# Kernel optimization log

Hardware: AMD Instinct MI355X
Metric: run time of the kernel (lower is better)

The kernel has to match this reference:

```python
import jax, jax.numpy as jnp
import numpy as np

NDIM = 1024
NHEAD = 16
HEAD_DIM = NDIM // NHEAD


def setup_inputs() -> dict:
    key = jax.random.key(0)
    ks = jax.random.split(key, 12)
    B, L, C = 2, 2048, NDIM
    s = 0.02
    return {
        "q": jax.random.normal(ks[0], (B, L, C), jnp.float32),
        "k": jax.random.normal(ks[1], (B, L, C), jnp.float32),
        "v": jax.random.normal(ks[2], (B, L, C), jnp.float32),
        "Wq": jax.random.normal(ks[3], (C, C), jnp.float32) * s,
        "bq": jax.random.normal(ks[4], (C,), jnp.float32) * s,
        "Wk": jax.random.normal(ks[5], (C, C), jnp.float32) * s,
        "bk": jax.random.normal(ks[6], (C,), jnp.float32) * s,
        "Wv": jax.random.normal(ks[7], (C, C), jnp.float32) * s,
        "bv": jax.random.normal(ks[8], (C,), jnp.float32) * s,
        "Wo": jax.random.normal(ks[9], (C, C), jnp.float32) * s,
        "bo": jax.random.normal(ks[10], (C,), jnp.float32) * s,
    }


def reference(q, k, v, Wq, bq, Wk, bk, Wv, bv, Wo, bo):
    B, Lq, C = q.shape
    H, D = NHEAD, HEAD_DIM
    # projections, then split heads: (B, H, L, D)
    qh = (q @ Wq + bq).reshape(B, Lq, H, D).transpose(0, 2, 1, 3)
    kh = (k @ Wk + bk).reshape(B, k.shape[1], H, D).transpose(0, 2, 1, 3)
    vh = (v @ Wv + bv).reshape(B, v.shape[1], H, D).transpose(0, 2, 1, 3)
    scale = 1.0 / jnp.sqrt(jnp.asarray(D, qh.dtype))
    att = jnp.einsum("bhqd,bhkd->bhqk", qh, kh) * scale  # (B,H,Lq,Lk)
    att = jax.nn.softmax(att, axis=-1)  # dropout p=0.0 -> identity
    y = jnp.einsum("bhqk,bhkd->bhqd", att, vh)
    y = y.transpose(0, 2, 1, 3).reshape(B, Lq, C)
    return y @ Wo + bo
```

## Files before the change

kernel.cpp:

```cpp
#include <hip/hip_runtime.h>
#include <math.h>

#define BATCH 2
#define SEQ   2048
#define CDIM  1024
#define NHEAD 16
#define HDIM  64
#define TOKS  (BATCH * SEQ)

typedef __bf16 bf16x8 __attribute__((ext_vector_type(8)));
typedef __bf16 bf16x2 __attribute__((ext_vector_type(2)));
typedef float  f32x4  __attribute__((ext_vector_type(4)));

#define MFMA16(a, b, c) __builtin_amdgcn_mfma_f32_16x16x32_bf16(a, b, c, 0, 0, 0)

#define QSCALE 0.1803368801111204f

__device__ __forceinline__ void gload_lds16(const __bf16* g, __bf16* l) {
    __builtin_amdgcn_global_load_lds(
        (const __attribute__((address_space(1))) unsigned int*)g,
        (__attribute__((address_space(3))) unsigned int*)l, 16, 0, 0);
}

__global__ __launch_bounds__(256) void prep_kernel(
    const float* __restrict__ q, const float* __restrict__ k, const float* __restrict__ v,
    __bf16* __restrict__ qo, __bf16* __restrict__ ko, __bf16* __restrict__ vo,
    const float* __restrict__ W0, const float* __restrict__ W1,
    const float* __restrict__ W2, const float* __restrict__ W3,
    __bf16* __restrict__ T0, __bf16* __restrict__ T1,
    __bf16* __restrict__ T2, __bf16* __restrict__ T3)
{
    __shared__ __bf16 Ts[64][72];
    const int bx = blockIdx.x;
    const int tid = threadIdx.x;

    if (bx < 6144) {
        const int t = bx >> 11;
        const size_t i = ((size_t)(bx & 2047) * 256 + tid) * 8;
        const float* s = t == 0 ? q : (t == 1 ? k : v);
        __bf16* d = t == 0 ? qo : (t == 1 ? ko : vo);
        const float4 x = *(const float4*)&s[i];
        const float4 y = *(const float4*)&s[i + 4];
        bf16x8 o;
        o[0] = (__bf16)x.x; o[1] = (__bf16)x.y; o[2] = (__bf16)x.z; o[3] = (__bf16)x.w;
        o[4] = (__bf16)y.x; o[5] = (__bf16)y.y; o[6] = (__bf16)y.z; o[7] = (__bf16)y.w;
        *(bf16x8*)&d[i] = o;
        return;
    }

    const int t  = bx - 6144;
    const int z  = t >> 8;
    const int ry = (t & 255) >> 4;
    const int rx = t & 15;
    const float* W = z == 0 ? W0 : z == 1 ? W1 : z == 2 ? W2 : W3;
    __bf16* T = z == 0 ? T0 : z == 1 ? T1 : z == 2 ? T2 : T3;
    const int rb = ry * 64, cb = rx * 64;
    const int r = tid >> 4;
    const int c4 = (tid & 15) * 4;
#pragma unroll
    for (int p = 0; p < 4; p++) {
        const int rr = p * 16 + r;
        const float4 w4 = *(const float4*)&W[(size_t)(rb + rr) * CDIM + cb + c4];
        Ts[c4 + 0][rr] = (__bf16)w4.x;
        Ts[c4 + 1][rr] = (__bf16)w4.y;
        Ts[c4 + 2][rr] = (__bf16)w4.z;
        Ts[c4 + 3][rr] = (__bf16)w4.w;
    }
    __syncthreads();
    const int n = tid >> 2;
    const int k16 = (tid & 3) * 16;
    *(bf16x8*)&T[(size_t)(cb + n) * CDIM + rb + k16]     = *(const bf16x8*)&Ts[n][k16];
    *(bf16x8*)&T[(size_t)(cb + n) * CDIM + rb + k16 + 8] = *(const bf16x8*)&Ts[n][k16 + 8];
}

__global__ __launch_bounds__(512, 6) void qkv_gemm_kernel(
    const __bf16* __restrict__ qb, const __bf16* __restrict__ kb,
    const __bf16* __restrict__ vb,
    const __bf16* __restrict__ Wqt, const __bf16* __restrict__ Wkt,
    const __bf16* __restrict__ Wvt,
    const float* __restrict__ bq, const float* __restrict__ bk,
    const float* __restrict__ bv,
    __bf16* __restrict__ Qh, __bf16* __restrict__ Kh, __bf16* __restrict__ Vht)
{
    __shared__ __bf16 As[128 * 32];
    __shared__ __bf16 Bs[128 * 32];

    const int lin = blockIdx.x + (blockIdx.y << 3) + (blockIdx.z << 8);
    const int nl  = (lin & 7) * 96 + (lin >> 3);
    const int bx  = nl & 7;
    const int by  = (nl >> 3) & 31;
    const int z   = nl >> 8;

    const __bf16* A    = z == 0 ? qb : z == 1 ? kb : Wvt;
    const __bf16* Bt   = z == 0 ? Wqt : z == 1 ? Wkt : vb;
    const float*  bias = z == 0 ? bq : z == 1 ? bk : bv;

    const int tid  = threadIdx.x;
    const int w    = tid >> 6;
    const int lane = tid & 63;
    const int quad = lane >> 4;
    const int c    = lane & 15;
    const int wm   = w >> 1;
    const int wn   = w & 1;
    const int rowBase = (z == 2 ? bx : by) * 128;
    const int colBase = (z == 2 ? by : bx) * 128;

    const int sr = lane >> 2;
    const int sk = (lane & 3) * 8;

    f32x4 acc[2][4];
#pragma unroll
    for (int i = 0; i < 2; i++)
#pragma unroll
        for (int j = 0; j < 4; j++) acc[i][j] = (f32x4){0, 0, 0, 0};

    const __bf16* srcA = A  + (size_t)(rowBase + w * 16 + sr) * CDIM + sk;
    const __bf16* srcB = Bt + (size_t)(colBase + w * 16 + sr) * CDIM + sk;
    __bf16* dstA = &As[w * 16 * 32];
    __bf16* dstB = &Bs[w * 16 * 32];

    for (int k0 = 0; k0 < CDIM; k0 += 32) {
        gload_lds16(srcA + k0, dstA);
        gload_lds16(srcB + k0, dstB);
        __syncthreads();

        bf16x8 af[2], bf[4];
#pragma unroll
        for (int i = 0; i < 2; i++)
            af[i] = *(const bf16x8*)&As[(wm * 32 + i * 16 + c) * 32 + quad * 8];
#pragma unroll
        for (int i = 0; i < 4; i++)
            bf[i] = *(const bf16x8*)&Bs[(wn * 64 + i * 16 + c) * 32 + quad * 8];
#pragma unroll
        for (int mi = 0; mi < 2; mi++)
#pragma unroll
            for (int ni = 0; ni < 4; ni++)
                acc[mi][ni] = MFMA16(af[mi], bf[ni], acc[mi][ni]);
        __syncthreads();
    }

#pragma unroll
    for (int mi = 0; mi < 2; mi++) {
#pragma unroll
        for (int ni = 0; ni < 4; ni++) {
            const int col = colBase + wn * 64 + ni * 16 + c;
#pragma unroll
            for (int r = 0; r < 4; r++) {
                const int row = rowBase + wm * 32 + mi * 16 + quad * 4 + r;
                const float val = acc[mi][ni][r];
                if (z == 2) {
                    const int col2 = (col & ~31) | (((col & 15) << 1) | ((col >> 4) & 1));
                    Vht[(size_t)row * TOKS + col2] = (__bf16)(val + bias[row]);
                } else {
                    const int b = row >> 11, l = row & 2047;
                    const int h = col >> 6,  d = col & 63;
                    const float s = (z == 0) ? QSCALE : 1.0f;
                    __bf16* outp = (z == 0) ? Qh : Kh;
                    outp[((((size_t)b * NHEAD + h) * SEQ) + l) * HDIM + d] =
                        (__bf16)((val + bias[col]) * s);
                }
            }
        }
    }
}

__global__ __launch_bounds__(512, 4) void out_gemm_kernel(
    const __bf16* __restrict__ A, const __bf16* __restrict__ Bt,
    const float* __restrict__ bias, float* __restrict__ out)
{
    __shared__ __bf16 As[128 * 32];
    __shared__ __bf16 Bs[64 * 32];

    const int lin = blockIdx.x + (blockIdx.y << 4);
    const int nl  = (lin & 7) * 64 + (lin >> 3);
    const int bx  = nl & 15;
    const int by  = nl >> 4;

    const int tid  = threadIdx.x;
    const int w    = tid >> 6;
    const int lane = tid & 63;
    const int quad = lane >> 4;
    const int c    = lane & 15;
    const int wm   = w >> 1;
    const int wn   = w & 1;
    const int rowBase = by * 128;
    const int colBase = bx * 64;
    const int sr = lane >> 2;
    const int sk = (lane & 3) * 8;

    f32x4 acc[2][2];
#pragma unroll
    for (int i = 0; i < 2; i++)
#pragma unroll
        for (int j = 0; j < 2; j++) acc[i][j] = (f32x4){0, 0, 0, 0};

    const __bf16* srcA = A + (size_t)(rowBase + w * 16 + sr) * CDIM + sk;
    const __bf16* srcB = Bt + (size_t)(colBase + (w & 3) * 16 + sr) * CDIM + sk;
    __bf16* dstA = &As[w * 16 * 32];
    __bf16* dstB = &Bs[(w & 3) * 16 * 32];

    for (int k0 = 0; k0 < CDIM; k0 += 32) {
        gload_lds16(srcA + k0, dstA);
        if (w < 4) gload_lds16(srcB + k0, dstB);
        __syncthreads();

        bf16x8 af[2], bf[2];
#pragma unroll
        for (int i = 0; i < 2; i++)
            af[i] = *(const bf16x8*)&As[(wm * 32 + i * 16 + c) * 32 + quad * 8];
#pragma unroll
        for (int i = 0; i < 2; i++)
            bf[i] = *(const bf16x8*)&Bs[(wn * 32 + i * 16 + c) * 32 + quad * 8];
#pragma unroll
        for (int mi = 0; mi < 2; mi++)
#pragma unroll
            for (int ni = 0; ni < 2; ni++)
                acc[mi][ni] = MFMA16(af[mi], bf[ni], acc[mi][ni]);
        __syncthreads();
    }

#pragma unroll
    for (int mi = 0; mi < 2; mi++) {
#pragma unroll
        for (int ni = 0; ni < 2; ni++) {
            const int col = colBase + wn * 32 + ni * 16 + c;
#pragma unroll
            for (int r = 0; r < 4; r++) {
                const int row = rowBase + wm * 32 + mi * 16 + quad * 4 + r;
                out[(size_t)row * CDIM + col] = acc[mi][ni][r] + bias[col];
            }
        }
    }
}

__global__ __launch_bounds__(256) void attn_v5_kernel(
    const __bf16* __restrict__ Qh, const __bf16* __restrict__ Kh,
    const __bf16* __restrict__ Vht, __bf16* __restrict__ Y)
{
    __shared__ __align__(16) __bf16 Ks[2][32][72];
    __shared__ __align__(16) __bf16 Vt[2][64][48];
    __shared__ __align__(16) unsigned int Pf[4][2][16][36];

    const int tid  = threadIdx.x;
    const int w    = tid >> 6;
    const int lane = tid & 63;
    const int quad = lane >> 4;
    const int c    = lane & 15;
    const int bh   = blockIdx.x;
    const int b    = bh >> 4;
    const int h    = bh & 15;
    const int qbase = blockIdx.y * 128 + w * 32;

    const __bf16* Qg = Qh + (size_t)bh * SEQ * HDIM;
    const __bf16* Kg = Kh + (size_t)bh * SEQ * HDIM;
    const __bf16* Vg = Vht + (size_t)(h * HDIM) * TOKS + (size_t)b * SEQ;

    bf16x8 qf[2][2];
#pragma unroll
    for (int g = 0; g < 2; g++) {
        qf[g][0] = *(const bf16x8*)&Qg[(size_t)(qbase + g * 16 + c) * HDIM + quad * 8];
        qf[g][1] = *(const bf16x8*)&Qg[(size_t)(qbase + g * 16 + c) * HDIM + 32 + quad * 8];
    }

    bf16x8 ones;
#pragma unroll
    for (int j = 0; j < 8; j++) ones[j] = (__bf16)1.0f;

    f32x4 O[2][4];
    f32x4 L[2];
#pragma unroll
    for (int g = 0; g < 2; g++) {
        L[g] = (f32x4){0, 0, 0, 0};
#pragma unroll
        for (int i = 0; i < 4; i++) O[g][i] = (f32x4){0, 0, 0, 0};
    }

    const int krow = tid >> 3, kcol = (tid & 7) * 8;
    const int vrow = tid >> 2, vcol = (tid & 3) * 8;

    {
        const bf16x8 k0 = *(const bf16x8*)&Kg[(size_t)krow * HDIM + kcol];
        const bf16x8 v0 = *(const bf16x8*)&Vg[(size_t)vrow * TOKS + vcol];
        *(bf16x8*)&Ks[0][krow][kcol] = k0;
        *(bf16x8*)&Vt[0][vrow][vcol] = v0;
    }
    __syncthreads();

    int buf = 0;
    for (int t0 = 0; t0 < SEQ; t0 += 32) {
        const int tn = t0 + 32;
        bf16x8 kpre, vpre;
        if (tn < SEQ) {
            kpre = *(const bf16x8*)&Kg[(size_t)(tn + krow) * HDIM + kcol];
            vpre = *(const bf16x8*)&Vg[(size_t)vrow * TOKS + tn + vcol];
        }

        const bf16x8 k00 = *(const bf16x8*)&Ks[buf][c][quad * 8];
        const bf16x8 k01 = *(const bf16x8*)&Ks[buf][c][32 + quad * 8];
        const bf16x8 k10 = *(const bf16x8*)&Ks[buf][16 + c][quad * 8];
        const bf16x8 k11 = *(const bf16x8*)&Ks[buf][16 + c][32 + quad * 8];
        const bf16x8 v0 = *(const bf16x8*)&Vt[buf][c][quad * 8];
        const bf16x8 v1 = *(const bf16x8*)&Vt[buf][16 + c][quad * 8];
        const bf16x8 v2 = *(const bf16x8*)&Vt[buf][32 + c][quad * 8];
        const bf16x8 v3 = *(const bf16x8*)&Vt[buf][48 + c][quad * 8];

#pragma unroll
        for (int g = 0; g < 2; g++) {
            f32x4 s0 = {0, 0, 0, 0}, s1 = {0, 0, 0, 0};
            s0 = MFMA16(qf[g][0], k00, s0);
            s0 = MFMA16(qf[g][1], k01, s0);
            s1 = MFMA16(qf[g][0], k10, s1);
            s1 = MFMA16(qf[g][1], k11, s1);
#pragma unroll
            for (int r = 0; r < 4; r++) {
                union { bf16x2 v; unsigned int u; } pk;
                pk.v[0] = (__bf16)__builtin_amdgcn_exp2f(s0[r]);
                pk.v[1] = (__bf16)__builtin_amdgcn_exp2f(s1[r]);
                Pf[w][g][quad * 4 + r][c] = pk.u;
            }
            const bf16x8 pf = *(const bf16x8*)&Pf[w][g][c][quad * 4];
            L[g]    = MFMA16(pf, ones, L[g]);
            O[g][0] = MFMA16(pf, v0, O[g][0]);
            O[g][1] = MFMA16(pf, v1, O[g][1]);
            O[g][2] = MFMA16(pf, v2, O[g][2]);
            O[g][3] = MFMA16(pf, v3, O[g][3]);
        }

        if (tn < SEQ) {
            *(bf16x8*)&Ks[buf ^ 1][krow][kcol] = kpre;
            *(bf16x8*)&Vt[buf ^ 1][vrow][vcol] = vpre;
        }
        __syncthreads();
        buf ^= 1;
    }

    __bf16* Yb = Y + (size_t)b * SEQ * CDIM;
#pragma unroll
    for (int g = 0; g < 2; g++) {
#pragma unroll
        for (int r = 0; r < 4; r++) {
            const float inv = 1.0f / L[g][r];
            const int l = qbase + g * 16 + quad * 4 + r;
            __bf16* yp = Yb + (size_t)l * CDIM + h * HDIM + c;
            yp[0]  = (__bf16)(O[g][0][r] * inv);
            yp[16] = (__bf16)(O[g][1][r] * inv);
            yp[32] = (__bf16)(O[g][2][r] * inv);
            yp[48] = (__bf16)(O[g][3][r] * inv);
        }
    }
}


extern "C" void kernel_launch(void* const* d_in, const int* in_sizes, int n_in,
                              void* d_out, int out_size, void* d_ws, size_t ws_size,
                              hipStream_t stream)
{
    const float* q  = (const float*)d_in[0];
    const float* k  = (const float*)d_in[1];
    const float* v  = (const float*)d_in[2];
    const float* Wq = (const float*)d_in[3];
    const float* bq = (const float*)d_in[4];
    const float* Wk = (const float*)d_in[5];
    const float* bk = (const float*)d_in[6];
    const float* Wv = (const float*)d_in[7];
    const float* bv = (const float*)d_in[8];
    const float* Wo = (const float*)d_in[9];
    const float* bo = (const float*)d_in[10];
    float* out = (float*)d_out;

    const size_t MAT = (size_t)TOKS * CDIM;
    const size_t WN  = (size_t)CDIM * CDIM;

    __bf16* p   = (__bf16*)d_ws;
    __bf16* qb  = p; p += MAT;
    __bf16* kb  = p; p += MAT;
    __bf16* vb  = p; p += MAT;
    __bf16* Wqt = p; p += WN;
    __bf16* Wkt = p; p += WN;
    __bf16* Wvt = p; p += WN;
    __bf16* Wot = p; p += WN;
    __bf16* Qh  = p; p += MAT;
    __bf16* Kh  = p; p += MAT;
    __bf16* Vht = p; p += MAT;
    __bf16* Yb  = qb;

    prep_kernel<<<dim3(7168), dim3(256), 0, stream>>>(
        q, k, v, qb, kb, vb, Wq, Wk, Wv, Wo, Wqt, Wkt, Wvt, Wot);

    qkv_gemm_kernel<<<dim3(8, 32, 3), dim3(512), 0, stream>>>(
        qb, kb, vb, Wqt, Wkt, Wvt, bq, bk, bv, Qh, Kh, Vht);

    attn_v5_kernel<<<dim3(BATCH * NHEAD, SEQ / 128), dim3(256), 0, stream>>>(Qh, Kh, Vht, Yb);

    out_gemm_kernel<<<dim3(16, 32), dim3(512), 0, stream>>>(Yb, Wot, bo, out);
}
```

Measured before the change: 225.4 us.

## Restructure attention to 8 waves of 16 query rows with 64-key tiles

The attention kernel now runs 512 threads per block. Each of 8 waves handles 16 query rows instead of 4 waves handling 32, and each iteration processes a 64-key tile instead of 32, halving the number of loop iterations and barriers. V fragments are loaded from LDS inside the PV loop, and s_setprio raises wave priority around the MFMA block. The goal is more waves for latency hiding and fewer syncs. The cost is that each wave reuses its K/V LDS reads across fewer query rows, and LDS use per block is larger.

```diff
diff --git a/kernel.cpp b/kernel.cpp
--- a/kernel.cpp
+++ b/kernel.cpp
@@ -233,13 +233,13 @@
     }
 }
 
-__global__ __launch_bounds__(256) void attn_v5_kernel(
+__global__ __launch_bounds__(512, 4) void attn_v6_kernel(
     const __bf16* __restrict__ Qh, const __bf16* __restrict__ Kh,
     const __bf16* __restrict__ Vht, __bf16* __restrict__ Y)
 {
-    __shared__ __align__(16) __bf16 Ks[2][32][72];
-    __shared__ __align__(16) __bf16 Vt[2][64][48];
-    __shared__ __align__(16) unsigned int Pf[4][2][16][36];
+    __shared__ __align__(16) __bf16 Ks[2][64][72];
+    __shared__ __align__(16) __bf16 Vt[2][64][72];
+    __shared__ __align__(16) unsigned int Pf[8][16][36];
 
     const int tid  = threadIdx.x;
     const int w    = tid >> 6;
@@ -249,86 +249,80 @@
     const int bh   = blockIdx.x;
     const int b    = bh >> 4;
     const int h    = bh & 15;
-    const int qbase = blockIdx.y * 128 + w * 32;
+    const int qbase = blockIdx.y * 128 + w * 16;
 
     const __bf16* Qg = Qh + (size_t)bh * SEQ * HDIM;
     const __bf16* Kg = Kh + (size_t)bh * SEQ * HDIM;
     const __bf16* Vg = Vht + (size_t)(h * HDIM) * TOKS + (size_t)b * SEQ;
 
-    bf16x8 qf[2][2];
-#pragma unroll
-    for (int g = 0; g < 2; g++) {
-        qf[g][0] = *(const bf16x8*)&Qg[(size_t)(qbase + g * 16 + c) * HDIM + quad * 8];
-        qf[g][1] = *(const bf16x8*)&Qg[(size_t)(qbase + g * 16 + c) * HDIM + 32 + quad * 8];
-    }
+    bf16x8 qf[2];
+    qf[0] = *(const bf16x8*)&Qg[(size_t)(qbase + c) * HDIM + quad * 8];
+    qf[1] = *(const bf16x8*)&Qg[(size_t)(qbase + c) * HDIM + 32 + quad * 8];
 
     bf16x8 ones;
 #pragma unroll
     for (int j = 0; j < 8; j++) ones[j] = (__bf16)1.0f;
 
-    f32x4 O[2][4];
-    f32x4 L[2];
-#pragma unroll
-    for (int g = 0; g < 2; g++) {
-        L[g] = (f32x4){0, 0, 0, 0};
-#pragma unroll
-        for (int i = 0; i < 4; i++) O[g][i] = (f32x4){0, 0, 0, 0};
-    }
-
-    const int krow = tid >> 3, kcol = (tid & 7) * 8;
-    const int vrow = tid >> 2, vcol = (tid & 3) * 8;
-
-    {
-        const bf16x8 k0 = *(const bf16x8*)&Kg[(size_t)krow * HDIM + kcol];
-        const bf16x8 v0 = *(const bf16x8*)&Vg[(size_t)vrow * TOKS + vcol];
-        *(bf16x8*)&Ks[0][krow][kcol] = k0;
-        *(bf16x8*)&Vt[0][vrow][vcol] = v0;
-    }
+    f32x4 O[4];
+    f32x4 L = (f32x4){0, 0, 0, 0};
+#pragma unroll
+    for (int i = 0; i < 4; i++) O[i] = (f32x4){0, 0, 0, 0};
+
+    const int srow = tid >> 3;
+    const int scol = (tid & 7) * 8;
+
+    *(bf16x8*)&Ks[0][srow][scol] = *(const bf16x8*)&Kg[(size_t)srow * HDIM + scol];
+    *(bf16x8*)&Vt[0][srow][scol] = *(const bf16x8*)&Vg[(size_t)srow * TOKS + scol];
     __syncthreads();
 
     int buf = 0;
-    for (int t0 = 0; t0 < SEQ; t0 += 32) {
-        const int tn = t0 + 32;
+    for (int t0 = 0; t0 < SEQ; t0 += 64) {
+        const int tn = t0 + 64;
         bf16x8 kpre, vpre;
         if (tn < SEQ) {
-            kpre = *(const bf16x8*)&Kg[(size_t)(tn + krow) * HDIM + kcol];
-            vpre = *(const bf16x8*)&Vg[(size_t)vrow * TOKS + tn + vcol];
-        }
-
-        const bf16x8 k00 = *(const bf16x8*)&Ks[buf][c][quad * 8];
-        const bf16x8 k01 = *(const bf16x8*)&Ks[buf][c][32 + quad * 8];
-        const bf16x8 k10 = *(const bf16x8*)&Ks[buf][16 + c][quad * 8];
-        const bf16x8 k11 = *(const bf16x8*)&Ks[buf][16 + c][32 + quad * 8];
-        const bf16x8 v0 = *(const bf16x8*)&Vt[buf][c][quad * 8];
-        const bf16x8 v1 = *(const bf16x8*)&Vt[buf][16 + c][quad * 8];
-        const bf16x8 v2 = *(const bf16x8*)&Vt[buf][32 + c][quad * 8];
-        const bf16x8 v3 = *(const bf16x8*)&Vt[buf][48 + c][quad * 8];
-
-#pragma unroll
-        for (int g = 0; g < 2; g++) {
-            f32x4 s0 = {0, 0, 0, 0}, s1 = {0, 0, 0, 0};
-            s0 = MFMA16(qf[g][0], k00, s0);
-            s0 = MFMA16(qf[g][1], k01, s0);
-            s1 = MFMA16(qf[g][0], k10, s1);
-            s1 = MFMA16(qf[g][1], k11, s1);
-#pragma unroll
-            for (int r = 0; r < 4; r++) {
-                union { bf16x2 v; unsigned int u; } pk;
-                pk.v[0] = (__bf16)__builtin_amdgcn_exp2f(s0[r]);
-                pk.v[1] = (__bf16)__builtin_amdgcn_exp2f(s1[r]);
-                Pf[w][g][quad * 4 + r][c] = pk.u;
-            }
-            const bf16x8 pf = *(const bf16x8*)&Pf[w][g][c][quad * 4];
-            L[g]    = MFMA16(pf, ones, L[g]);
-            O[g][0] = MFMA16(pf, v0, O[g][0]);
-            O[g][1] = MFMA16(pf, v1, O[g][1]);
-            O[g][2] = MFMA16(pf, v2, O[g][2]);
-            O[g][3] = MFMA16(pf, v3, O[g][3]);
-        }
+            kpre = *(const bf16x8*)&Kg[(size_t)(tn + srow) * HDIM + scol];
+            vpre = *(const bf16x8*)&Vg[(size_t)srow * TOKS + tn + scol];
+        }
+
+        f32x4 s[4];
+#pragma unroll
+        for (int j = 0; j < 4; j++) {
+            const bf16x8 k0 = *(const bf16x8*)&Ks[buf][j * 16 + c][quad * 8];
+            const bf16x8 k1 = *(const bf16x8*)&Ks[buf][j * 16 + c][32 + quad * 8];
+            f32x4 t = {0, 0, 0, 0};
+            t = MFMA16(qf[0], k0, t);
+            t = MFMA16(qf[1], k1, t);
+            s[j] = t;
+        }
+
+#pragma unroll
+        for (int r = 0; r < 4; r++) {
+            union { bf16x2 v; unsigned int u; } pa, pb;
+            pa.v[0] = (__bf16)__builtin_amdgcn_exp2f(s[0][r]);
+            pa.v[1] = (__bf16)__builtin_amdgcn_exp2f(s[1][r]);
+            pb.v[0] = (__bf16)__builtin_amdgcn_exp2f(s[2][r]);
+            pb.v[1] = (__bf16)__builtin_amdgcn_exp2f(s[3][r]);
+            Pf[w][quad * 4 + r][c]      = pa.u;
+            Pf[w][quad * 4 + r][16 + c] = pb.u;
+        }
+        const bf16x8 pf0 = *(const bf16x8*)&Pf[w][c][quad * 4];
+        const bf16x8 pf1 = *(const bf16x8*)&Pf[w][c][16 + quad * 4];
+
+        __builtin_amdgcn_s_setprio(1);
+        L = MFMA16(pf0, ones, L);
+        L = MFMA16(pf1, ones, L);
+#pragma unroll
+        for (int i = 0; i < 4; i++) {
+            const bf16x8 vA = *(const bf16x8*)&Vt[buf][16 * i + c][quad * 8];
+            const bf16x8 vB = *(const bf16x8*)&Vt[buf][16 * i + c][32 + quad * 8];
+            O[i] = MFMA16(pf0, vA, O[i]);
+            O[i] = MFMA16(pf1, vB, O[i]);
+        }
+        __builtin_amdgcn_s_setprio(0);
 
         if (tn < SEQ) {
-            *(bf16x8*)&Ks[buf ^ 1][krow][kcol] = kpre;
-            *(bf16x8*)&Vt[buf ^ 1][vrow][vcol] = vpre;
+            *(bf16x8*)&Ks[buf ^ 1][srow][scol] = kpre;
+            *(bf16x8*)&Vt[buf ^ 1][srow][scol] = vpre;
         }
         __syncthreads();
         buf ^= 1;
@@ -336,17 +330,14 @@
 
     __bf16* Yb = Y + (size_t)b * SEQ * CDIM;
 #pragma unroll
-    for (int g = 0; g < 2; g++) {
-#pragma unroll
-        for (int r = 0; r < 4; r++) {
-            const float inv = 1.0f / L[g][r];
-            const int l = qbase + g * 16 + quad * 4 + r;
-            __bf16* yp = Yb + (size_t)l * CDIM + h * HDIM + c;
-            yp[0]  = (__bf16)(O[g][0][r] * inv);
-            yp[16] = (__bf16)(O[g][1][r] * inv);
-            yp[32] = (__bf16)(O[g][2][r] * inv);
-            yp[48] = (__bf16)(O[g][3][r] * inv);
-        }
+    for (int r = 0; r < 4; r++) {
+        const float inv = 1.0f / L[r];
+        const int l = qbase + quad * 4 + r;
+        __bf16* yp = Yb + (size_t)l * CDIM + h * HDIM + c;
+        yp[0]  = (__bf16)(O[0][r] * inv);
+        yp[16] = (__bf16)(O[1][r] * inv);
+        yp[32] = (__bf16)(O[2][r] * inv);
+        yp[48] = (__bf16)(O[3][r] * inv);
     }
 }
 
@@ -390,7 +381,7 @@
     qkv_gemm_kernel<<<dim3(8, 32, 3), dim3(512), 0, stream>>>(
         qb, kb, vb, Wqt, Wkt, Wvt, bq, bk, bv, Qh, Kh, Vht);
 
-    attn_v5_kernel<<<dim3(BATCH * NHEAD, SEQ / 128), dim3(256), 0, stream>>>(Qh, Kh, Vht, Yb);
+    attn_v6_kernel<<<dim3(BATCH * NHEAD, SEQ / 128), dim3(512), 0, stream>>>(Qh, Kh, Vht, Yb);
 
     out_gemm_kernel<<<dim3(16, 32), dim3(512), 0, stream>>>(Yb, Wot, bo, out);
 }
```

New measurement: 225.5 us. Within noise of the previous version (+0.0%).
